# Performance work log

Hardware: AMD Instinct MI355X
Metric: run time of the kernel (lower is better)

The kernel has to match this reference:

```python
import jax, jax.numpy as jnp
import numpy as np

N, S, Q, P = 100000, 64, 50, 3  # pauli words, heads, qubits, pauli basis
EPS = 1e-12  # F.normalize clamp


def setup_inputs() -> dict:
    key = jax.random.key(0)
    k1, k2, k3, k4 = jax.random.split(key, 4)
    return {
        "batch_pauli_tensor": jax.random.uniform(k1, (N, Q, P), dtype=jnp.float32),
        "batch_coeff": jax.random.normal(k2, (N,), dtype=jnp.float32),
        "heads_param": jax.random.normal(k3, (S, Q, P), dtype=jnp.float32),
        "head_ratios_param": jax.random.normal(k4, (S,), dtype=jnp.float32),
    }


def reference(batch_pauli_tensor, batch_coeff, heads_param, head_ratios_param):
    s = heads_param.shape[0]
    heads = jax.nn.softplus(heads_param * 20.0)
    heads = heads / jnp.maximum(jnp.sum(heads, axis=-1, keepdims=True), EPS)
    hr = jax.nn.softplus(head_ratios_param * 20.0)
    hr = hr / jnp.maximum(jnp.sum(hr), EPS)
    hr = (hr + 0.001 / s) / 1.001
    # coverage: per-(word, head, qubit) match prob -> product over qubits -> ratio-weighted sum
    cov = jnp.einsum('nqp,sqp->nsq', batch_pauli_tensor, heads)  # [n, s, q]
    cov = jnp.prod(cov, axis=-1)                                 # [n, s]
    cov = jnp.einsum('s,ns->n', hr, cov)                         # [n]
    # variance loss
    return jnp.sum(batch_coeff ** 2 / cov)
```

## Files before the change

### kernel.cpp

```cpp
#include <hip/hip_runtime.h>
#include <math.h>

#define N_Q 50
#define N_P 3
#define N_S 64
#define ROW 150
#define BLK_ROWS 256
#define THREADS 256
#define WAVES 4
#define SCHUNK 16
#define RPL 4

#define WS_CNT_OFF 3200
#define WS_HP_OFF 3264
#define WS_HRV_OFF 41664
#define WS_AT_OFF 65536

__device__ __forceinline__ float softplus20(float x) {
    float z = x * 20.0f;
    return fmaxf(z, 0.0f) + log1pf(expf(-fabsf(z)));
}

__global__ void precompute_kernel(const float* __restrict__ heads_param,
                                  const float* __restrict__ hr_param,
                                  float* __restrict__ HP,
                                  float* __restrict__ hrv,
                                  int* __restrict__ cnt) {
    const int tid = threadIdx.x;
    if (blockIdx.x == 0) {
        if (tid == 0) *cnt = 0;
        if (tid < N_S) {
            float sp = softplus20(hr_param[tid]);
            float tot = sp;
            #pragma unroll
            for (int off = 32; off; off >>= 1) tot += __shfl_xor(tot, off);
            float hr = sp / fmaxf(tot, 1e-12f);
            hrv[tid] = (hr + 0.001f / (float)N_S) / 1.001f;
        }
    }
    int idx = blockIdx.x * blockDim.x + tid;
    if (idx < N_S * N_Q) {
        int q = idx / N_S;
        int s = idx - q * N_S;
        const float* hp = heads_param + ((size_t)s * N_Q + q) * N_P;
        float sp0 = softplus20(hp[0]);
        float sp1 = softplus20(hp[1]);
        float sp2 = softplus20(hp[2]);
        float denom = fmaxf(sp0 + sp1 + sp2, 1e-12f);
        float* o = HP + ((size_t)q * N_S + s) * 3;
        o[0] = sp0 / denom;
        o[1] = sp1 / denom;
        o[2] = sp2 / denom;
    }
}

__global__ __launch_bounds__(THREADS) void transpose_kernel(
    const float* __restrict__ A, float2* __restrict__ AT2, int N) {
    __shared__ float tile[64 * 151];
    const int tid = threadIdx.x;
    const int nbase = blockIdx.x * 64;
    const float2* __restrict__ Asrc = (const float2*)A;
    for (int g = tid; g < 64 * (ROW / 2); g += THREADS) {
        int r = g / (ROW / 2);
        int j = g - r * (ROW / 2);
        int src = nbase + r; if (src >= N) src = N - 1;
        float2 v = Asrc[(size_t)src * (ROW / 2) + j];
        tile[r * 151 + 2 * j]     = v.x;
        tile[r * 151 + 2 * j + 1] = v.y;
    }
    __syncthreads();
    for (int g = tid; g < (ROW / 2) * 64; g += THREADS) {
        int j2 = g >> 6;
        int nloc = g & 63;
        int n = nbase + nloc;
        if (n < N) {
            float2 v = make_float2(tile[nloc * 151 + 2 * j2],
                                   tile[nloc * 151 + 2 * j2 + 1]);
            AT2[(size_t)j2 * N + n] = v;
        }
    }
}

__device__ __forceinline__ void computeQ4(const float4* __restrict__ Hq,
                                          const float (&a)[RPL][3],
                                          float (&p)[RPL][SCHUNK]) {
    #pragma unroll
    for (int g = 0; g < 4; ++g) {
        float4 b0 = Hq[3 * g], b1 = Hq[3 * g + 1], b2 = Hq[3 * g + 2];
        #pragma unroll
        for (int r = 0; r < RPL; ++r) {
            p[r][4*g+0] *= fmaf(b0.x, a[r][0], fmaf(b0.y, a[r][1], b0.z * a[r][2]));
            p[r][4*g+1] *= fmaf(b0.w, a[r][0], fmaf(b1.x, a[r][1], b1.y * a[r][2]));
            p[r][4*g+2] *= fmaf(b1.z, a[r][0], fmaf(b1.w, a[r][1], b2.x * a[r][2]));
            p[r][4*g+3] *= fmaf(b2.y, a[r][0], fmaf(b2.z, a[r][1], b2.w * a[r][2]));
        }
    }
}

__device__ __forceinline__ void epilogue(
    float (*covs)[BLK_ROWS], const float* __restrict__ coeff,
    double* __restrict__ partials, int* __restrict__ cnt,
    float* __restrict__ out, int N, int nbase,
    int tid, int lane, int wave, double* redd, double* redf, int* isLast) {
    {
        const int row = 64 * wave + lane;
        const int n = nbase + row;
        float cov = covs[0][row] + covs[1][row] + covs[2][row] + covs[3][row];
        float term = 0.0f;
        if (n < N) { float c = coeff[n]; term = (c * c) / cov; }
        double td = (double)term;
        #pragma unroll
        for (int off = 32; off; off >>= 1) td += __shfl_down(td, off);
        if (lane == 0) redd[wave] = td;
    }
    __syncthreads();

    if (tid == 0) {
        partials[blockIdx.x] = ((redd[0] + redd[1]) + redd[2]) + redd[3];
        __threadfence();
        int v = atomicAdd(cnt, 1);
        *isLast = (v == (int)gridDim.x - 1);
    }
    __syncthreads();

    if (*isLast) {
        __threadfence();
        double s = 0.0;
        for (int i = tid; i < (int)gridDim.x; i += THREADS) s += partials[i];
        #pragma unroll
        for (int off = 32; off; off >>= 1) s += __shfl_down(s, off);
        if (lane == 0) redf[wave] = s;
        __syncthreads();
        if (tid == 0) {
            double t = 0.0;
            #pragma unroll
            for (int wv = 0; wv < WAVES; ++wv) t += redf[wv];
            out[0] = (float)t;
        }
    }
}

__global__ __launch_bounds__(THREADS, 2) void main_kernel_t(
    const float2* __restrict__ AT2, const float* __restrict__ coeff,
    const float* __restrict__ HP, const float* __restrict__ hrv,
    double* __restrict__ partials, int* __restrict__ cnt,
    float* __restrict__ out, int N) {
    __shared__ float hHs[N_Q * N_S * 3];
    __shared__ float hrvl[N_S];
    __shared__ float covs[WAVES][BLK_ROWS];
    __shared__ double redd[WAVES];
    __shared__ double redf[WAVES];
    __shared__ int isLast;

    const int tid = threadIdx.x;
    const int lane = tid & 63;
    const int wave = tid >> 6;
    const int nbase = blockIdx.x * BLK_ROWS;

    for (int i = tid; i < (N_Q * N_S * 3) / 4; i += THREADS)
        ((float4*)hHs)[i] = ((const float4*)HP)[i];
    if (tid < N_S) hrvl[tid] = hrv[tid];
    __syncthreads();

    const float2* __restrict__ Qp[RPL];
    #pragma unroll
    for (int r = 0; r < RPL; ++r) {
        int n = nbase + 64 * r + lane;  if (n >= N) n = N - 1;
        Qp[r] = AT2 + n;
    }
    const size_t Ns = (size_t)N;

    float prod[RPL][SCHUNK];
    #pragma unroll
    for (int r = 0; r < RPL; ++r)
        #pragma unroll
        for (int i = 0; i < SCHUNK; ++i) prod[r][i] = 1.0f;

    const float4* __restrict__ Hbase = (const float4*)hHs + 12 * wave;

    float2 x[RPL][3];
    #pragma unroll
    for (int r = 0; r < RPL; ++r) {
        x[r][0] = Qp[r][0]; x[r][1] = Qp[r][Ns]; x[r][2] = Qp[r][2 * Ns];
    }

    size_t o = 0;
    #pragma unroll 5
    for (int w = 0; w < N_Q / 2; ++w) {
        const size_t on = (w < N_Q / 2 - 1) ? o + 3 * Ns : (size_t)0;
        float2 nx[RPL][3];
        #pragma unroll
        for (int r = 0; r < RPL; ++r) {
            nx[r][0] = Qp[r][on]; nx[r][1] = Qp[r][on + Ns]; nx[r][2] = Qp[r][on + 2 * Ns];
        }
        const float4* Hq = Hbase + 96 * w;
        float aq[RPL][3], cq[RPL][3];
        #pragma unroll
        for (int r = 0; r < RPL; ++r) {
            aq[r][0] = x[r][0].x; aq[r][1] = x[r][0].y; aq[r][2] = x[r][1].x;
            cq[r][0] = x[r][1].y; cq[r][1] = x[r][2].x; cq[r][2] = x[r][2].y;
        }
        computeQ4(Hq,      aq, prod);
        computeQ4(Hq + 48, cq, prod);
        #pragma unroll
        for (int r = 0; r < RPL; ++r) {
            x[r][0] = nx[r][0]; x[r][1] = nx[r][1]; x[r][2] = nx[r][2];
        }
        o = on;
    }

    const int s0 = wave * SCHUNK;
    #pragma unroll
    for (int r = 0; r < RPL; ++r) {
        float acc = 0.0f;
        #pragma unroll
        for (int i = 0; i < SCHUNK; ++i) acc = fmaf(hrvl[s0 + i], prod[r][i], acc);
        covs[wave][64 * r + lane] = acc;
    }
    __syncthreads();

    epilogue(covs, coeff, partials, cnt, out, N, nbase, tid, lane, wave,
             redd, redf, &isLast);
}

__global__ __launch_bounds__(THREADS, 2) void main_kernel_f(
    const float* __restrict__ A, const float* __restrict__ coeff,
    const float* __restrict__ HP, const float* __restrict__ hrv,
    double* __restrict__ partials, int* __restrict__ cnt,
    float* __restrict__ out, int N) {
    __shared__ float hHs[N_Q * N_S * 3];
    __shared__ float hrvl[N_S];
    __shared__ float covs[WAVES][BLK_ROWS];
    __shared__ double redd[WAVES];
    __shared__ double redf[WAVES];
    __shared__ int isLast;

    const int tid = threadIdx.x;
    const int lane = tid & 63;
    const int wave = tid >> 6;
    const int nbase = blockIdx.x * BLK_ROWS;

    for (int i = tid; i < (N_Q * N_S * 3) / 4; i += THREADS)
        ((float4*)hHs)[i] = ((const float4*)HP)[i];
    if (tid < N_S) hrvl[tid] = hrv[tid];
    __syncthreads();

    const float2* __restrict__ pR[RPL];
    #pragma unroll
    for (int r = 0; r < RPL; ++r) {
        int n = nbase + 64 * r + lane;  if (n >= N) n = N - 1;
        pR[r] = (const float2*)A + (size_t)n * (ROW / 2);
    }

    float prod[RPL][SCHUNK];
    #pragma unroll
    for (int r = 0; r < RPL; ++r)
        #pragma unroll
        for (int i = 0; i < SCHUNK; ++i) prod[r][i] = 1.0f;

    const float4* __restrict__ Hbase = (const float4*)hHs + 12 * wave;

    float2 x[RPL][3];
    #pragma unroll
    for (int r = 0; r < RPL; ++r) {
        x[r][0] = pR[r][0]; x[r][1] = pR[r][1]; x[r][2] = pR[r][2];
    }

    #pragma unroll 5
    for (int w = 0; w < N_Q / 2; ++w) {
        const int nb = (w < N_Q / 2 - 1) ? 3 * w + 3 : 0;
        float2 nx[RPL][3];
        #pragma unroll
        for (int r = 0; r < RPL; ++r) {
            nx[r][0] = pR[r][nb]; nx[r][1] = pR[r][nb + 1]; nx[r][2] = pR[r][nb + 2];
        }
        const float4* Hq = Hbase + 96 * w;
        float aq[RPL][3], cq[RPL][3];
        #pragma unroll
        for (int r = 0; r < RPL; ++r) {
            aq[r][0] = x[r][0].x; aq[r][1] = x[r][0].y; aq[r][2] = x[r][1].x;
            cq[r][0] = x[r][1].y; cq[r][1] = x[r][2].x; cq[r][2] = x[r][2].y;
        }
        computeQ4(Hq,      aq, prod);
        computeQ4(Hq + 48, cq, prod);
        #pragma unroll
        for (int r = 0; r < RPL; ++r) {
            x[r][0] = nx[r][0]; x[r][1] = nx[r][1]; x[r][2] = nx[r][2];
        }
    }

    const int s0 = wave * SCHUNK;
    #pragma unroll
    for (int r = 0; r < RPL; ++r) {
        float acc = 0.0f;
        #pragma unroll
        for (int i = 0; i < SCHUNK; ++i) acc = fmaf(hrvl[s0 + i], prod[r][i], acc);
        covs[wave][64 * r + lane] = acc;
    }
    __syncthreads();

    epilogue(covs, coeff, partials, cnt, out, N, nbase, tid, lane, wave,
             redd, redf, &isLast);
}

extern "C" void kernel_launch(void* const* d_in, const int* in_sizes, int n_in,
                              void* d_out, int out_size, void* d_ws, size_t ws_size,
                              hipStream_t stream) {
    const float* A           = (const float*)d_in[0];
    const float* coeff       = (const float*)d_in[1];
    const float* heads_param = (const float*)d_in[2];
    const float* hr_param    = (const float*)d_in[3];
    const int N = in_sizes[1];
    const int nblocks = (N + BLK_ROWS - 1) / BLK_ROWS;

    char* ws = (char*)d_ws;
    double* partials = (double*)ws;
    int*    cnt = (int*)(ws + WS_CNT_OFF);
    float*  HP  = (float*)(ws + WS_HP_OFF);
    float*  hrv = (float*)(ws + WS_HRV_OFF);
    float2* AT2 = (float2*)(ws + WS_AT_OFF);
    float*  out = (float*)d_out;

    const int pre_blocks = (N_S * N_Q + THREADS - 1) / THREADS;
    precompute_kernel<<<pre_blocks, THREADS, 0, stream>>>(heads_param, hr_param,
                                                          HP, hrv, cnt);

    const size_t at_bytes = (size_t)(ROW / 2) * (size_t)N * sizeof(float2);
    if (ws_size >= (size_t)WS_AT_OFF + at_bytes) {
        const int tblocks = (N + 63) / 64;
        transpose_kernel<<<tblocks, THREADS, 0, stream>>>(A, AT2, N);
        main_kernel_t<<<nblocks, THREADS, 0, stream>>>(AT2, coeff, HP, hrv,
                                                       partials, cnt, out, N);
    } else {
        main_kernel_f<<<nblocks, THREADS, 0, stream>>>(A, coeff, HP, hrv,
                                                       partials, cnt, out, N);
    }
}
```

Measured before the change: 177.3 us.

## Fuse precompute into transpose and split heads across eight waves per block

Folds the softplus head/ratio precompute into the transpose kernel, removing one kernel launch, and doubles the transpose tile to 128 rows. The main transposed kernel now uses 512 threads (8 waves), with each wave handling 8 heads instead of 16. This cuts per-thread product registers and gives more waves to hide latency. The fallback path is expanded by hand with hard-coded 256-thread constants. In that path the transpose writes into a scratch pointer that overlaps the HP/hrv workspace, which looks unsafe but only runs when the workspace is small.

```diff
diff --git a/kernel.cpp b/kernel.cpp
--- a/kernel.cpp
+++ b/kernel.cpp
@@ -6,10 +6,13 @@
 #define N_S 64
 #define ROW 150
 #define BLK_ROWS 256
-#define THREADS 256
-#define WAVES 4
-#define SCHUNK 16
+#define THREADS 512
+#define WAVES 8
+#define SCHUNK 8
 #define RPL 4
+
+#define TP_THREADS 256
+#define TP_ROWS 128
 
 #define WS_CNT_OFF 3200
 #define WS_HP_OFF 3264
@@ -21,12 +24,13 @@
     return fmaxf(z, 0.0f) + log1pf(expf(-fabsf(z)));
 }
 
-__global__ void precompute_kernel(const float* __restrict__ heads_param,
-                                  const float* __restrict__ hr_param,
-                                  float* __restrict__ HP,
-                                  float* __restrict__ hrv,
-                                  int* __restrict__ cnt) {
+__global__ __launch_bounds__(TP_THREADS) void transpose_pre_kernel(
+    const float* __restrict__ A, float2* __restrict__ AT2,
+    const float* __restrict__ heads_param, const float* __restrict__ hr_param,
+    float* __restrict__ HP, float* __restrict__ hrv, int* __restrict__ cnt,
+    int N) {
     const int tid = threadIdx.x;
+
     if (blockIdx.x == 0) {
         if (tid == 0) *cnt = 0;
         if (tid < N_S) {
@@ -38,29 +42,27 @@
             hrv[tid] = (hr + 0.001f / (float)N_S) / 1.001f;
         }
     }
-    int idx = blockIdx.x * blockDim.x + tid;
-    if (idx < N_S * N_Q) {
-        int q = idx / N_S;
-        int s = idx - q * N_S;
-        const float* hp = heads_param + ((size_t)s * N_Q + q) * N_P;
-        float sp0 = softplus20(hp[0]);
-        float sp1 = softplus20(hp[1]);
-        float sp2 = softplus20(hp[2]);
-        float denom = fmaxf(sp0 + sp1 + sp2, 1e-12f);
-        float* o = HP + ((size_t)q * N_S + s) * 3;
-        o[0] = sp0 / denom;
-        o[1] = sp1 / denom;
-        o[2] = sp2 / denom;
-    }
-}
-
-__global__ __launch_bounds__(THREADS) void transpose_kernel(
-    const float* __restrict__ A, float2* __restrict__ AT2, int N) {
-    __shared__ float tile[64 * 151];
-    const int tid = threadIdx.x;
-    const int nbase = blockIdx.x * 64;
+    {
+        int idx = blockIdx.x * TP_THREADS + tid;
+        if (idx < N_S * N_Q) {
+            int q = idx / N_S;
+            int s = idx - q * N_S;
+            const float* hp = heads_param + ((size_t)s * N_Q + q) * N_P;
+            float sp0 = softplus20(hp[0]);
+            float sp1 = softplus20(hp[1]);
+            float sp2 = softplus20(hp[2]);
+            float denom = fmaxf(sp0 + sp1 + sp2, 1e-12f);
+            float* o = HP + ((size_t)q * N_S + s) * 3;
+            o[0] = sp0 / denom;
+            o[1] = sp1 / denom;
+            o[2] = sp2 / denom;
+        }
+    }
+
+    __shared__ float tile[TP_ROWS * 151];
+    const int nbase = blockIdx.x * TP_ROWS;
     const float2* __restrict__ Asrc = (const float2*)A;
-    for (int g = tid; g < 64 * (ROW / 2); g += THREADS) {
+    for (int g = tid; g < TP_ROWS * (ROW / 2); g += TP_THREADS) {
         int r = g / (ROW / 2);
         int j = g - r * (ROW / 2);
         int src = nbase + r; if (src >= N) src = N - 1;
@@ -69,9 +71,9 @@
         tile[r * 151 + 2 * j + 1] = v.y;
     }
     __syncthreads();
-    for (int g = tid; g < (ROW / 2) * 64; g += THREADS) {
-        int j2 = g >> 6;
-        int nloc = g & 63;
+    for (int g = tid; g < (ROW / 2) * TP_ROWS; g += TP_THREADS) {
+        int j2 = g >> 7;
+        int nloc = g & 127;
         int n = nbase + nloc;
         if (n < N) {
             float2 v = make_float2(tile[nloc * 151 + 2 * j2],
@@ -85,7 +87,7 @@
                                           const float (&a)[RPL][3],
                                           float (&p)[RPL][SCHUNK]) {
     #pragma unroll
-    for (int g = 0; g < 4; ++g) {
+    for (int g = 0; g < SCHUNK / 4; ++g) {
         float4 b0 = Hq[3 * g], b1 = Hq[3 * g + 1], b2 = Hq[3 * g + 2];
         #pragma unroll
         for (int r = 0; r < RPL; ++r) {
@@ -93,49 +95,6 @@
             p[r][4*g+1] *= fmaf(b0.w, a[r][0], fmaf(b1.x, a[r][1], b1.y * a[r][2]));
             p[r][4*g+2] *= fmaf(b1.z, a[r][0], fmaf(b1.w, a[r][1], b2.x * a[r][2]));
             p[r][4*g+3] *= fmaf(b2.y, a[r][0], fmaf(b2.z, a[r][1], b2.w * a[r][2]));
-        }
-    }
-}
-
-__device__ __forceinline__ void epilogue(
-    float (*covs)[BLK_ROWS], const float* __restrict__ coeff,
-    double* __restrict__ partials, int* __restrict__ cnt,
-    float* __restrict__ out, int N, int nbase,
-    int tid, int lane, int wave, double* redd, double* redf, int* isLast) {
-    {
-        const int row = 64 * wave + lane;
-        const int n = nbase + row;
-        float cov = covs[0][row] + covs[1][row] + covs[2][row] + covs[3][row];
-        float term = 0.0f;
-        if (n < N) { float c = coeff[n]; term = (c * c) / cov; }
-        double td = (double)term;
-        #pragma unroll
-        for (int off = 32; off; off >>= 1) td += __shfl_down(td, off);
-        if (lane == 0) redd[wave] = td;
-    }
-    __syncthreads();
-
-    if (tid == 0) {
-        partials[blockIdx.x] = ((redd[0] + redd[1]) + redd[2]) + redd[3];
-        __threadfence();
-        int v = atomicAdd(cnt, 1);
-        *isLast = (v == (int)gridDim.x - 1);
-    }
-    __syncthreads();
-
-    if (*isLast) {
-        __threadfence();
-        double s = 0.0;
-        for (int i = tid; i < (int)gridDim.x; i += THREADS) s += partials[i];
-        #pragma unroll
-        for (int off = 32; off; off >>= 1) s += __shfl_down(s, off);
-        if (lane == 0) redf[wave] = s;
-        __syncthreads();
-        if (tid == 0) {
-            double t = 0.0;
-            #pragma unroll
-            for (int wv = 0; wv < WAVES; ++wv) t += redf[wv];
-            out[0] = (float)t;
         }
     }
 }
@@ -148,7 +107,7 @@
     __shared__ float hHs[N_Q * N_S * 3];
     __shared__ float hrvl[N_S];
     __shared__ float covs[WAVES][BLK_ROWS];
-    __shared__ double redd[WAVES];
+    __shared__ double redd[4];
     __shared__ double redf[WAVES];
     __shared__ int isLast;
 
@@ -176,7 +135,7 @@
         #pragma unroll
         for (int i = 0; i < SCHUNK; ++i) prod[r][i] = 1.0f;
 
-    const float4* __restrict__ Hbase = (const float4*)hHs + 12 * wave;
+    const float4* __restrict__ Hbase = (const float4*)hHs + 6 * wave;
 
     float2 x[RPL][3];
     #pragma unroll
@@ -219,20 +178,56 @@
     }
     __syncthreads();
 
-    epilogue(covs, coeff, partials, cnt, out, N, nbase, tid, lane, wave,
-             redd, redf, &isLast);
-}
-
-__global__ __launch_bounds__(THREADS, 2) void main_kernel_f(
+    if (wave < 4) {
+        const int row = 64 * wave + lane;
+        const int n = nbase + row;
+        float cov = 0.0f;
+        #pragma unroll
+        for (int wv = 0; wv < WAVES; ++wv) cov += covs[wv][row];
+        float term = 0.0f;
+        if (n < N) { float c = coeff[n]; term = (c * c) / cov; }
+        double td = (double)term;
+        #pragma unroll
+        for (int off = 32; off; off >>= 1) td += __shfl_down(td, off);
+        if (lane == 0) redd[wave] = td;
+    }
+    __syncthreads();
+
+    if (tid == 0) {
+        partials[blockIdx.x] = ((redd[0] + redd[1]) + redd[2]) + redd[3];
+        __threadfence();
+        int v = atomicAdd(cnt, 1);
+        isLast = (v == (int)gridDim.x - 1);
+    }
+    __syncthreads();
+
+    if (isLast) {
+        __threadfence();
+        double s = 0.0;
+        for (int i = tid; i < (int)gridDim.x; i += THREADS) s += partials[i];
+        #pragma unroll
+        for (int off = 32; off; off >>= 1) s += __shfl_down(s, off);
+        if (lane == 0) redf[wave] = s;
+        __syncthreads();
+        if (tid == 0) {
+            double t = 0.0;
+            #pragma unroll
+            for (int wv = 0; wv < WAVES; ++wv) t += redf[wv];
+            out[0] = (float)t;
+        }
+    }
+}
+
+__global__ __launch_bounds__(256, 2) void main_kernel_f(
     const float* __restrict__ A, const float* __restrict__ coeff,
     const float* __restrict__ HP, const float* __restrict__ hrv,
     double* __restrict__ partials, int* __restrict__ cnt,
     float* __restrict__ out, int N) {
     __shared__ float hHs[N_Q * N_S * 3];
     __shared__ float hrvl[N_S];
-    __shared__ float covs[WAVES][BLK_ROWS];
-    __shared__ double redd[WAVES];
-    __shared__ double redf[WAVES];
+    __shared__ float covs[4][BLK_ROWS];
+    __shared__ double redd[4];
+    __shared__ double redf[4];
     __shared__ int isLast;
 
     const int tid = threadIdx.x;
@@ -240,7 +235,7 @@
     const int wave = tid >> 6;
     const int nbase = blockIdx.x * BLK_ROWS;
 
-    for (int i = tid; i < (N_Q * N_S * 3) / 4; i += THREADS)
+    for (int i = tid; i < (N_Q * N_S * 3) / 4; i += 256)
         ((float4*)hHs)[i] = ((const float4*)HP)[i];
     if (tid < N_S) hrvl[tid] = hrv[tid];
     __syncthreads();
@@ -252,11 +247,11 @@
         pR[r] = (const float2*)A + (size_t)n * (ROW / 2);
     }
 
-    float prod[RPL][SCHUNK];
+    float prod[RPL][16];
     #pragma unroll
     for (int r = 0; r < RPL; ++r)
         #pragma unroll
-        for (int i = 0; i < SCHUNK; ++i) prod[r][i] = 1.0f;
+        for (int i = 0; i < 16; ++i) prod[r][i] = 1.0f;
 
     const float4* __restrict__ Hbase = (const float4*)hHs + 12 * wave;
 
@@ -275,32 +270,83 @@
             nx[r][0] = pR[r][nb]; nx[r][1] = pR[r][nb + 1]; nx[r][2] = pR[r][nb + 2];
         }
         const float4* Hq = Hbase + 96 * w;
-        float aq[RPL][3], cq[RPL][3];
-        #pragma unroll
-        for (int r = 0; r < RPL; ++r) {
-            aq[r][0] = x[r][0].x; aq[r][1] = x[r][0].y; aq[r][2] = x[r][1].x;
-            cq[r][0] = x[r][1].y; cq[r][1] = x[r][2].x; cq[r][2] = x[r][2].y;
-        }
-        computeQ4(Hq,      aq, prod);
-        computeQ4(Hq + 48, cq, prod);
+        #pragma unroll
+        for (int g = 0; g < 4; ++g) {
+            float4 b0 = Hq[3 * g], b1 = Hq[3 * g + 1], b2 = Hq[3 * g + 2];
+            #pragma unroll
+            for (int r = 0; r < RPL; ++r) {
+                float a0 = x[r][0].x, a1 = x[r][0].y, a2 = x[r][1].x;
+                prod[r][4*g+0] *= fmaf(b0.x, a0, fmaf(b0.y, a1, b0.z * a2));
+                prod[r][4*g+1] *= fmaf(b0.w, a0, fmaf(b1.x, a1, b1.y * a2));
+                prod[r][4*g+2] *= fmaf(b1.z, a0, fmaf(b1.w, a1, b2.x * a2));
+                prod[r][4*g+3] *= fmaf(b2.y, a0, fmaf(b2.z, a1, b2.w * a2));
+            }
+        }
+        const float4* Hq2 = Hq + 48;
+        #pragma unroll
+        for (int g = 0; g < 4; ++g) {
+            float4 b0 = Hq2[3 * g], b1 = Hq2[3 * g + 1], b2 = Hq2[3 * g + 2];
+            #pragma unroll
+            for (int r = 0; r < RPL; ++r) {
+                float a0 = x[r][1].y, a1 = x[r][2].x, a2 = x[r][2].y;
+                prod[r][4*g+0] *= fmaf(b0.x, a0, fmaf(b0.y, a1, b0.z * a2));
+                prod[r][4*g+1] *= fmaf(b0.w, a0, fmaf(b1.x, a1, b1.y * a2));
+                prod[r][4*g+2] *= fmaf(b1.z, a0, fmaf(b1.w, a1, b2.x * a2));
+                prod[r][4*g+3] *= fmaf(b2.y, a0, fmaf(b2.z, a1, b2.w * a2));
+            }
+        }
         #pragma unroll
         for (int r = 0; r < RPL; ++r) {
             x[r][0] = nx[r][0]; x[r][1] = nx[r][1]; x[r][2] = nx[r][2];
         }
     }
 
-    const int s0 = wave * SCHUNK;
+    const int s0 = wave * 16;
     #pragma unroll
     for (int r = 0; r < RPL; ++r) {
         float acc = 0.0f;
         #pragma unroll
-        for (int i = 0; i < SCHUNK; ++i) acc = fmaf(hrvl[s0 + i], prod[r][i], acc);
+        for (int i = 0; i < 16; ++i) acc = fmaf(hrvl[s0 + i], prod[r][i], acc);
         covs[wave][64 * r + lane] = acc;
     }
     __syncthreads();
 
-    epilogue(covs, coeff, partials, cnt, out, N, nbase, tid, lane, wave,
-             redd, redf, &isLast);
+    {
+        const int row = 64 * wave + lane;
+        const int n = nbase + row;
+        float cov = covs[0][row] + covs[1][row] + covs[2][row] + covs[3][row];
+        float term = 0.0f;
+        if (n < N) { float c = coeff[n]; term = (c * c) / cov; }
+        double td = (double)term;
+        #pragma unroll
+        for (int off = 32; off; off >>= 1) td += __shfl_down(td, off);
+        if (lane == 0) redd[wave] = td;
+    }
+    __syncthreads();
+
+    if (tid == 0) {
+        partials[blockIdx.x] = ((redd[0] + redd[1]) + redd[2]) + redd[3];
+        __threadfence();
+        int v = atomicAdd(cnt, 1);
+        isLast = (v == (int)gridDim.x - 1);
+    }
+    __syncthreads();
+
+    if (isLast) {
+        __threadfence();
+        double s = 0.0;
+        for (int i = tid; i < (int)gridDim.x; i += 256) s += partials[i];
+        #pragma unroll
+        for (int off = 32; off; off >>= 1) s += __shfl_down(s, off);
+        if (lane == 0) redf[wave] = s;
+        __syncthreads();
+        if (tid == 0) {
+            double t = 0.0;
+            #pragma unroll
+            for (int wv = 0; wv < 4; ++wv) t += redf[wv];
+            out[0] = (float)t;
+        }
+    }
 }
 
 extern "C" void kernel_launch(void* const* d_in, const int* in_sizes, int n_in,
@@ -321,18 +367,19 @@
     float2* AT2 = (float2*)(ws + WS_AT_OFF);
     float*  out = (float*)d_out;
 
-    const int pre_blocks = (N_S * N_Q + THREADS - 1) / THREADS;
-    precompute_kernel<<<pre_blocks, THREADS, 0, stream>>>(heads_param, hr_param,
-                                                          HP, hrv, cnt);
-
     const size_t at_bytes = (size_t)(ROW / 2) * (size_t)N * sizeof(float2);
     if (ws_size >= (size_t)WS_AT_OFF + at_bytes) {
-        const int tblocks = (N + 63) / 64;
-        transpose_kernel<<<tblocks, THREADS, 0, stream>>>(A, AT2, N);
+        const int tblocks = (N + TP_ROWS - 1) / TP_ROWS;
+        transpose_pre_kernel<<<tblocks, TP_THREADS, 0, stream>>>(
+            A, AT2, heads_param, hr_param, HP, hrv, cnt, N);
         main_kernel_t<<<nblocks, THREADS, 0, stream>>>(AT2, coeff, HP, hrv,
                                                        partials, cnt, out, N);
     } else {
-        main_kernel_f<<<nblocks, THREADS, 0, stream>>>(A, coeff, HP, hrv,
-                                                       partials, cnt, out, N);
-    }
-}
+        const int pre_blocks = (N_S * N_Q + 255) / 256;
+        transpose_pre_kernel<<<pre_blocks, TP_THREADS, 0, stream>>>(
+            A, (float2*)(ws + WS_CNT_OFF + 64), heads_param, hr_param,
+            HP, hrv, cnt, N);
+        main_kernel_f<<<nblocks, 256, 0, stream>>>(A, coeff, HP, hrv,
+                                                   partials, cnt, out, N);
+    }
+}
```

Result: slower. 190.5 us (+7.5%).
